# Kernel optimization log

Hardware: AMD Instinct MI355X
Metric: run time of the kernel (lower is better)

Reference implementation:

```python
import jax, jax.numpy as jnp
import numpy as np

WINDOW_SIZE = 11
SIGMA = 1.5
CHANNELS = 3
WEIGHT = 0.1
DATA_RANGE = 1.0


def _gaussian_kernel(window_size, sigma, channels):
    coords = jnp.arange(window_size, dtype=jnp.float32) - window_size // 2
    g = jnp.exp(-coords ** 2 / (2.0 * sigma ** 2))
    g = g / g.sum()
    k2d = jnp.outer(g, g)  # (W, W)
    # OIHW depthwise kernel: (channels, 1, W, W)
    return jnp.tile(k2d[None, None, :, :], (channels, 1, 1, 1))


def _dwconv(x, window):
    pad = WINDOW_SIZE // 2
    return jax.lax.conv_general_dilated(
        x, window,
        window_strides=(1, 1),
        padding=[(pad, pad), (pad, pad)],
        dimension_numbers=("NCHW", "OIHW", "NCHW"),
        feature_group_count=CHANNELS,
    )


def setup_inputs() -> dict:
    key = jax.random.key(0)
    k1, k2 = jax.random.split(key)
    shape = (16, 3, 512, 512)
    pred = jax.random.uniform(k1, shape, dtype=jnp.float32)
    target = jax.random.uniform(k2, shape, dtype=jnp.float32)
    window = _gaussian_kernel(WINDOW_SIZE, SIGMA, CHANNELS)
    return {"pred": pred, "target": target, "window": window}


def reference(pred, target, window):
    C1 = (0.01 * DATA_RANGE) ** 2
    C2 = (0.03 * DATA_RANGE) ** 2
    mu1 = _dwconv(pred, window)
    mu2 = _dwconv(target, window)
    mu1_sq = mu1 * mu1
    mu2_sq = mu2 * mu2
    mu1_mu2 = mu1 * mu2
    sigma1_sq = _dwconv(pred * pred, window) - mu1_sq
    sigma2_sq = _dwconv(target * target, window) - mu2_sq
    sigma12 = _dwconv(pred * target, window) - mu1_mu2
    numerator = (2.0 * mu1_mu2 + C1) * (2.0 * sigma12 + C2)
    denominator = (mu1_sq + mu2_sq + C1) * (sigma1_sq + sigma2_sq + C2)
    ssim_val = jnp.mean(numerator / denominator)
    return WEIGHT * (1.0 - ssim_val)
```

## Files before the change

### kernel.cpp

```cpp
#include <hip/hip_runtime.h>

typedef _Float16 half8 __attribute__((ext_vector_type(8)));
typedef _Float16 half4 __attribute__((ext_vector_type(4)));
typedef float f32x4 __attribute__((ext_vector_type(4)));

#define W 512
#define H 512
#define NPIX (16.0f*3.0f*512.0f*512.0f)
#define NACC 64
#define TPSTR 88
#define TPL (64*TPSTR)
#define ROWF 84
#define TOFF 6720
#define SFLOATS 13568
#define NT 12
#define NSLOT 7
#define NINST 53

#define VMCNT0() asm volatile("s_waitcnt vmcnt(0)" ::: "memory")
#define LGKM0()  asm volatile("s_waitcnt lgkmcnt(0)" ::: "memory")
#define BAR()    { asm volatile("" ::: "memory"); __builtin_amdgcn_s_barrier(); asm volatile("" ::: "memory"); }

__global__ __launch_bounds__(512) void ssim_main(const float* __restrict__ pred,
                                                 const float* __restrict__ targ,
                                                 const float* __restrict__ win,
                                                 float* __restrict__ ws) {
    const int tid  = threadIdx.x;
    const int lane = tid & 63;
    const int wv   = tid >> 6;
    const int lo   = lane & 15;
    const int hi   = lane >> 4;

    float* acc = ws;
    const float* zp = ws + 64;

    __shared__ __align__(16) float stageA[SFLOATS];
    __shared__ __align__(16) float stageB[SFLOATS];
    __shared__ __align__(16) _Float16 TP[4 * TPL];
    __shared__ _Float16 gw[64];
    __shared__ float wsum[8];

    if (tid < 64) {
        const int d = tid - 18;
        float val = 0.f;
        if (d >= 0 && d <= 10)
            val = win[55 + d] * __builtin_amdgcn_rcpf(sqrtf(win[60]));
        gw[tid] = (_Float16)val;
    }
    __syncthreads();

    half8 Bw;
    #pragma unroll
    for (int j = 0; j < 8; ++j)
        Bw[j] = gw[15 + hi * 8 + j - lo];

    int prow[NSLOT], pcol[NSLOT], parr[NSLOT];
    #pragma unroll
    for (int s = 0; s < NSLOT; ++s) {
        const int inst = s * 8 + wv;
        const int id   = inst * 64 + lane;
        const int arr  = (id >= 1680) ? 1 : 0;
        const int cid  = id - arr * 1680;
        const int r    = (cid * 3121) >> 16;
        const int cc   = cid - r * 21;
        const bool bad = (r >= 80) || (cc >= 20);
        prow[s] = bad ? 0x100000 : r;
        pcol[s] = cc * 4 - 8;
        parr[s] = arr;
    }

    const int b  = (blockIdx.x & 7) * 32 + (blockIdx.x >> 3);
    const int t0 = b * NT;
    float sum = 0.f;
    const f32x4 zero4 = {0.f, 0.f, 0.f, 0.f};
    const float C1 = 1e-4f, C2 = 9e-4f;

#define STAGE(tidx, BUF)                                                       \
    {                                                                          \
        const int nc = (tidx) >> 6, rem = (tidx) & 63;                         \
        const int y0 = (rem >> 3) * 64, x0 = (rem & 7) * 64;                   \
        const float* P  = pred + (size_t)nc * (W * H);                         \
        const float* Tt = targ + (size_t)nc * (W * H);                         \
        _Pragma("unroll")                                                      \
        for (int s = 0; s < NSLOT; ++s) {                                      \
            const int inst = s * 8 + wv;                                       \
            if (inst < NINST) {                                                \
                const int gy = y0 - 8 + prow[s];                               \
                const int gx = x0 + pcol[s];                                   \
                const bool ok = ((unsigned)gy < H) && ((unsigned)gx < W);      \
                const float* bp  = parr[s] ? Tt : P;                           \
                const float* src = ok ? (bp + (gy * W + gx)) : zp;             \
                __builtin_amdgcn_global_load_lds(                              \
                    (const __attribute__((address_space(1))) void*)src,        \
                    (__attribute__((address_space(3))) void*)&BUF[inst * 256], \
                    16, 0, 0);                                                 \
            }                                                                  \
        }                                                                      \
        __builtin_amdgcn_sched_barrier(0);            \
    }

#define COMPUTE(BUF)                                                           \
    {                                                                          \
        _Pragma("unroll")                                                      \
        for (int it = 0; it < 3; ++it) {                                       \
            const int t = wv + it * 8;                                         \
            if (t < 20) {                                                      \
                const int rt = t >> 2, ct = t & 3;                             \
                const int row  = rt * 16 + lo;                                 \
                const int coff = ct * 16 + hi * 8;                             \
                const float* SP = &BUF[row * ROWF + coff];                     \
                float pf[8], tf[8];                                            \
                *(float4*)&pf[0] = *(const float4*)SP;                         \
                *(float4*)&pf[4] = *(const float4*)(SP + 4);                   \
                *(float4*)&tf[0] = *(const float4*)(SP + TOFF);                \
                *(float4*)&tf[4] = *(const float4*)(SP + TOFF + 4);            \
                half8 pa, ta, qa, xa;                                          \
                _Pragma("unroll")                                              \
                for (int j = 0; j < 8; ++j) {                                  \
                    const float p = pf[j], t2 = tf[j];                         \
                    pa[j] = (_Float16)p;                                       \
                    ta[j] = (_Float16)t2;                                      \
                    qa[j] = (_Float16)fmaf(t2, t2, p * p);                     \
                    xa[j] = (_Float16)(p * t2);                                \
                }                                                              \
                const f32x4 d0 = __builtin_amdgcn_mfma_f32_16x16x32_f16(pa, Bw, zero4, 0, 0, 0); \
                const f32x4 d1 = __builtin_amdgcn_mfma_f32_16x16x32_f16(ta, Bw, zero4, 0, 0, 0); \
                const f32x4 d2 = __builtin_amdgcn_mfma_f32_16x16x32_f16(qa, Bw, zero4, 0, 0, 0); \
                const f32x4 d3 = __builtin_amdgcn_mfma_f32_16x16x32_f16(xa, Bw, zero4, 0, 0, 0); \
                const int tbase = (ct * 16 + lo) * TPSTR + rt * 16 + hi * 4;   \
                half4 h0, h1, h2, h3;                                          \
                _Pragma("unroll")                                              \
                for (int r = 0; r < 4; ++r) {                                  \
                    h0[r] = (_Float16)d0[r]; h1[r] = (_Float16)d1[r];          \
                    h2[r] = (_Float16)d2[r]; h3[r] = (_Float16)d3[r];          \
                }                                                              \
                *(half4*)&TP[0 * TPL + tbase] = h0;                            \
                *(half4*)&TP[1 * TPL + tbase] = h1;                            \
                *(half4*)&TP[2 * TPL + tbase] = h2;                            \
                *(half4*)&TP[3 * TPL + tbase] = h3;                            \
            }                                                                  \
        }                                                                      \
        LGKM0(); BAR();                                                        \
        _Pragma("unroll")                                                      \
        for (int iv = 0; iv < 2; ++iv) {                                       \
            const int v = wv + iv * 8;                                         \
            const int rtv = v >> 2, ct = v & 3;                                \
            const int abase = (ct * 16 + lo) * TPSTR + rtv * 16 + hi * 8;      \
            const half8 a0 = *(const half8*)&TP[0 * TPL + abase];              \
            const half8 a1 = *(const half8*)&TP[1 * TPL + abase];              \
            const half8 a2 = *(const half8*)&TP[2 * TPL + abase];              \
            const half8 a3 = *(const half8*)&TP[3 * TPL + abase];              \
            const f32x4 m1 = __builtin_amdgcn_mfma_f32_16x16x32_f16(a0, Bw, zero4, 0, 0, 0); \
            const f32x4 m2 = __builtin_amdgcn_mfma_f32_16x16x32_f16(a1, Bw, zero4, 0, 0, 0); \
            const f32x4 qq = __builtin_amdgcn_mfma_f32_16x16x32_f16(a2, Bw, zero4, 0, 0, 0); \
            const f32x4 pt = __builtin_amdgcn_mfma_f32_16x16x32_f16(a3, Bw, zero4, 0, 0, 0); \
            _Pragma("unroll")                                                  \
            for (int r = 0; r < 4; ++r) {                                      \
                const float mu1 = m1[r], mu2 = m2[r];                          \
                const float ms  = fmaf(mu1, mu1, mu2 * mu2);                   \
                const float m12 = mu1 * mu2;                                   \
                const float s12 = pt[r] - m12;                                 \
                const float ssm = qq[r] - ms;                                  \
                const float num = fmaf(2.f, m12, C1) * fmaf(2.f, s12, C2);     \
                const float den = (ms + C1) * (ssm + C2);                      \
                sum += num * __builtin_amdgcn_rcpf(den);                       \
            }                                                                  \
        }                                                                      \
    }

    STAGE(t0, stageA);
    VMCNT0(); BAR();

    #pragma unroll 1
    for (int i = 0; i < NT; i += 2) {
        STAGE(t0 + i + 1, stageB);
        COMPUTE(stageA);
        VMCNT0(); BAR();
        if (i + 2 < NT) STAGE(t0 + i + 2, stageA);
        COMPUTE(stageB);
        VMCNT0(); BAR();
    }

    #pragma unroll
    for (int off = 32; off > 0; off >>= 1) sum += __shfl_down(sum, off, 64);
    if (lane == 0) wsum[wv] = sum;
    __syncthreads();
    if (tid == 0) {
        float bs = 0.f;
        #pragma unroll
        for (int w2 = 0; w2 < 8; ++w2) bs += wsum[w2];
        atomicAdd(&acc[blockIdx.x & (NACC - 1)], bs);
    }
#undef STAGE
#undef COMPUTE
}

__global__ void ssim_final(const float* __restrict__ acc, float* __restrict__ out) {
    float s = 0.f;
    #pragma unroll
    for (int i = 0; i < NACC; ++i) s += acc[i];
    out[0] = 0.1f * (1.0f - s / NPIX);
}

extern "C" void kernel_launch(void* const* d_in, const int* in_sizes, int n_in,
                              void* d_out, int out_size, void* d_ws, size_t ws_size,
                              hipStream_t stream) {
    const float* pred = (const float*)d_in[0];
    const float* targ = (const float*)d_in[1];
    const float* win  = (const float*)d_in[2];
    float* out = (float*)d_out;
    float* ws  = (float*)d_ws;

    hipMemsetAsync(ws, 0, 512, stream);
    ssim_main<<<256, 512, 0, stream>>>(pred, targ, win, ws);
    ssim_final<<<1, 1, 0, stream>>>(ws, out);
}
```

Before: 40.62 us.

## Halve tile width to 64x32, use 256-thread blocks and 512 blocks

```diff
diff --git a/kernel.cpp b/kernel.cpp
--- a/kernel.cpp
+++ b/kernel.cpp
@@ -8,20 +8,19 @@
 #define H 512
 #define NPIX (16.0f*3.0f*512.0f*512.0f)
 #define NACC 64
-#define TPSTR 88
-#define TPL (64*TPSTR)
-#define ROWF 84
-#define TOFF 6720
-#define SFLOATS 13568
+#define AFL 3696
+#define SFL 7424
+#define NINST 29
+#define TPSTR 80
+#define TPL 2560
 #define NT 12
-#define NSLOT 7
-#define NINST 53
 
 #define VMCNT0() asm volatile("s_waitcnt vmcnt(0)" ::: "memory")
 #define LGKM0()  asm volatile("s_waitcnt lgkmcnt(0)" ::: "memory")
 #define BAR()    { asm volatile("" ::: "memory"); __builtin_amdgcn_s_barrier(); asm volatile("" ::: "memory"); }
-
-__global__ __launch_bounds__(512) void ssim_main(const float* __restrict__ pred,
+#define MFMA(A,B) __builtin_amdgcn_mfma_f32_16x16x32_f16((A),(B),zero4,0,0,0)
+
+__global__ __launch_bounds__(256) void ssim_main(const float* __restrict__ pred,
                                                  const float* __restrict__ targ,
                                                  const float* __restrict__ win,
                                                  float* __restrict__ ws) {
@@ -34,11 +33,10 @@
     float* acc = ws;
     const float* zp = ws + 64;
 
-    __shared__ __align__(16) float stageA[SFLOATS];
-    __shared__ __align__(16) float stageB[SFLOATS];
-    __shared__ __align__(16) _Float16 TP[4 * TPL];
+    __shared__ float stageA[SFL];
+    __shared__ float stageB[SFL];
+    __shared__ _Float16 TP[4 * TPL];
     __shared__ _Float16 gw[64];
-    __shared__ float wsum[8];
 
     if (tid < 64) {
         const int d = tid - 18;
@@ -47,49 +45,50 @@
             val = win[55 + d] * __builtin_amdgcn_rcpf(sqrtf(win[60]));
         gw[tid] = (_Float16)val;
     }
-    __syncthreads();
-
-    half8 Bw;
-    #pragma unroll
-    for (int j = 0; j < 8; ++j)
-        Bw[j] = gw[15 + hi * 8 + j - lo];
-
-    int prow[NSLOT], pcol[NSLOT], parr[NSLOT];
-    #pragma unroll
-    for (int s = 0; s < NSLOT; ++s) {
-        const int inst = s * 8 + wv;
+    {
+        const half4 z4 = {(_Float16)0.f, (_Float16)0.f, (_Float16)0.f, (_Float16)0.f};
+        #pragma unroll
+        for (int i = 0; i < 10; ++i)
+            *(half4*)&TP[(i * 256 + tid) * 4] = z4;
+    }
+
+    int prow[8], pcol[8], parr[8];
+    #pragma unroll
+    for (int s = 0; s < 8; ++s) {
+        const int inst = s * 4 + wv;
         const int id   = inst * 64 + lane;
-        const int arr  = (id >= 1680) ? 1 : 0;
-        const int cid  = id - arr * 1680;
-        const int r    = (cid * 3121) >> 16;
-        const int cc   = cid - r * 21;
-        const bool bad = (r >= 80) || (cc >= 20);
-        prow[s] = bad ? 0x100000 : r;
+        const bool okid = (id < 1848);
+        const int arr  = (id >= 924 && okid) ? 1 : 0;
+        const int cid  = id - 924 * arr;
+        const int r    = (cid * 5462) >> 16;
+        const int cc   = cid - r * 12;
+        prow[s] = okid ? r : (1 << 20);
         pcol[s] = cc * 4 - 8;
         parr[s] = arr;
     }
 
-    const int b  = (blockIdx.x & 7) * 32 + (blockIdx.x >> 3);
-    const int t0 = b * NT;
-    float sum = 0.f;
     const f32x4 zero4 = {0.f, 0.f, 0.f, 0.f};
     const float C1 = 1e-4f, C2 = 9e-4f;
+    float sum = 0.f;
+
+    const int bsw = (blockIdx.x & 7) * 64 + (blockIdx.x >> 3);
+    const int t0  = bsw * NT;
 
 #define STAGE(tidx, BUF)                                                       \
     {                                                                          \
-        const int nc = (tidx) >> 6, rem = (tidx) & 63;                         \
-        const int y0 = (rem >> 3) * 64, x0 = (rem & 7) * 64;                   \
-        const float* P  = pred + (size_t)nc * (W * H);                         \
-        const float* Tt = targ + (size_t)nc * (W * H);                         \
+        const int nc = (tidx) >> 7, rem = (tidx) & 127;                        \
+        const int y0 = (rem >> 4) * 64, x0 = (rem & 15) * 32;                  \
+        const float* Pb = pred + (size_t)nc * (W * H);                         \
+        const float* Tb = targ + (size_t)nc * (W * H);                         \
         _Pragma("unroll")                                                      \
-        for (int s = 0; s < NSLOT; ++s) {                                      \
-            const int inst = s * 8 + wv;                                       \
-            if (inst < NINST) {                                                \
+        for (int s = 0; s < 8; ++s) {                                          \
+            const int inst = s * 4 + wv;                                       \
+            if (inst < NINST) {                              \
                 const int gy = y0 - 8 + prow[s];                               \
                 const int gx = x0 + pcol[s];                                   \
                 const bool ok = ((unsigned)gy < H) && ((unsigned)gx < W);      \
-                const float* bp  = parr[s] ? Tt : P;                           \
-                const float* src = ok ? (bp + (gy * W + gx)) : zp;             \
+                const float* bp  = parr[s] ? Tb : Pb;                          \
+                const float* src = ok ? (bp + ((size_t)gy * W + gx)) : zp;     \
                 __builtin_amdgcn_global_load_lds(                              \
                     (const __attribute__((address_space(1))) void*)src,        \
                     (__attribute__((address_space(3))) void*)&BUF[inst * 256], \
@@ -103,57 +102,61 @@
     {                                                                          \
         _Pragma("unroll")                                                      \
         for (int it = 0; it < 3; ++it) {                                       \
-            const int t = wv + it * 8;                                         \
-            if (t < 20) {                                                      \
-                const int rt = t >> 2, ct = t & 3;                             \
-                const int row  = rt * 16 + lo;                                 \
-                const int coff = ct * 16 + hi * 8;                             \
-                const float* SP = &BUF[row * ROWF + coff];                     \
+            const int t = wv + it * 4;                                         \
+            if (t < 10) {                                    \
+                const int rt = t >> 1, ct = t & 1;                             \
+                const float* SP = &BUF[(rt * 16 + lo) * 48 + ct * 16 + hi * 8];\
                 float pf[8], tf[8];                                            \
-                *(float4*)&pf[0] = *(const float4*)SP;                         \
-                *(float4*)&pf[4] = *(const float4*)(SP + 4);                   \
-                *(float4*)&tf[0] = *(const float4*)(SP + TOFF);                \
-                *(float4*)&tf[4] = *(const float4*)(SP + TOFF + 4);            \
-                half8 pa, ta, qa, xa;                                          \
+                *(f32x4*)&pf[0] = *(const f32x4*)SP;                           \
+                *(f32x4*)&pf[4] = *(const f32x4*)(SP + 4);                     \
+                *(f32x4*)&tf[0] = *(const f32x4*)(SP + AFL);                   \
+                *(f32x4*)&tf[4] = *(const f32x4*)(SP + AFL + 4);               \
+                half8 pa, ta;                                                  \
                 _Pragma("unroll")                                              \
                 for (int j = 0; j < 8; ++j) {                                  \
-                    const float p = pf[j], t2 = tf[j];                         \
-                    pa[j] = (_Float16)p;                                       \
-                    ta[j] = (_Float16)t2;                                      \
-                    qa[j] = (_Float16)fmaf(t2, t2, p * p);                     \
-                    xa[j] = (_Float16)(p * t2);                                \
+                    pa[j] = (_Float16)pf[j];                                   \
+                    ta[j] = (_Float16)tf[j];                                   \
                 }                                                              \
-                const f32x4 d0 = __builtin_amdgcn_mfma_f32_16x16x32_f16(pa, Bw, zero4, 0, 0, 0); \
-                const f32x4 d1 = __builtin_amdgcn_mfma_f32_16x16x32_f16(ta, Bw, zero4, 0, 0, 0); \
-                const f32x4 d2 = __builtin_amdgcn_mfma_f32_16x16x32_f16(qa, Bw, zero4, 0, 0, 0); \
-                const f32x4 d3 = __builtin_amdgcn_mfma_f32_16x16x32_f16(xa, Bw, zero4, 0, 0, 0); \
-                const int tbase = (ct * 16 + lo) * TPSTR + rt * 16 + hi * 4;   \
-                half4 h0, h1, h2, h3;                                          \
-                _Pragma("unroll")                                              \
-                for (int r = 0; r < 4; ++r) {                                  \
-                    h0[r] = (_Float16)d0[r]; h1[r] = (_Float16)d1[r];          \
-                    h2[r] = (_Float16)d2[r]; h3[r] = (_Float16)d3[r];          \
+                const half8 qa = pa * pa + ta * ta;                            \
+                const half8 xa = pa * ta;                                      \
+                const f32x4 d0 = MFMA(pa, Bw);                                 \
+                const f32x4 d1 = MFMA(ta, Bw);                                 \
+                const f32x4 d2 = MFMA(qa, Bw);                                 \
+                const f32x4 d3 = MFMA(xa, Bw);                                 \
+                const int tb = (ct * 16 + lo) * TPSTR + rt * 16 + hi * 4;      \
+                if (rt == 4 && hi == 3) {          \
+                    TP[0 * TPL + tb] = (_Float16)d0[0];                        \
+                    TP[1 * TPL + tb] = (_Float16)d1[0];                        \
+                    TP[2 * TPL + tb] = (_Float16)d2[0];                        \
+                    TP[3 * TPL + tb] = (_Float16)d3[0];                        \
+                } else {                                                       \
+                    half4 h0, h1, h2, h3;                                      \
+                    _Pragma("unroll")                                          \
+                    for (int r = 0; r < 4; ++r) {                              \
+                        h0[r] = (_Float16)d0[r]; h1[r] = (_Float16)d1[r];      \
+                        h2[r] = (_Float16)d2[r]; h3[r] = (_Float16)d3[r];      \
+                    }                                                          \
+                    *(half4*)&TP[0 * TPL + tb] = h0;                           \
+                    *(half4*)&TP[1 * TPL + tb] = h1;                           \
+                    *(half4*)&TP[2 * TPL + tb] = h2;                           \
+                    *(half4*)&TP[3 * TPL + tb] = h3;                           \
                 }                                                              \
-                *(half4*)&TP[0 * TPL + tbase] = h0;                            \
-                *(half4*)&TP[1 * TPL + tbase] = h1;                            \
-                *(half4*)&TP[2 * TPL + tbase] = h2;                            \
-                *(half4*)&TP[3 * TPL + tbase] = h3;                            \
             }                                                                  \
         }                                                                      \
-        LGKM0(); BAR();                                                        \
+        LGKM0(); BAR();                      \
         _Pragma("unroll")                                                      \
         for (int iv = 0; iv < 2; ++iv) {                                       \
-            const int v = wv + iv * 8;                                         \
-            const int rtv = v >> 2, ct = v & 3;                                \
-            const int abase = (ct * 16 + lo) * TPSTR + rtv * 16 + hi * 8;      \
-            const half8 a0 = *(const half8*)&TP[0 * TPL + abase];              \
-            const half8 a1 = *(const half8*)&TP[1 * TPL + abase];              \
-            const half8 a2 = *(const half8*)&TP[2 * TPL + abase];              \
-            const half8 a3 = *(const half8*)&TP[3 * TPL + abase];              \
-            const f32x4 m1 = __builtin_amdgcn_mfma_f32_16x16x32_f16(a0, Bw, zero4, 0, 0, 0); \
-            const f32x4 m2 = __builtin_amdgcn_mfma_f32_16x16x32_f16(a1, Bw, zero4, 0, 0, 0); \
-            const f32x4 qq = __builtin_amdgcn_mfma_f32_16x16x32_f16(a2, Bw, zero4, 0, 0, 0); \
-            const f32x4 pt = __builtin_amdgcn_mfma_f32_16x16x32_f16(a3, Bw, zero4, 0, 0, 0); \
+            const int v = wv + iv * 4;                                         \
+            const int rtv = v >> 1, ct = v & 1;                                \
+            const int ah = (ct * 16 + lo) * TPSTR + rtv * 16 + hi * 8;         \
+            const half8 a0 = *(const half8*)&TP[0 * TPL + ah];                 \
+            const half8 a1 = *(const half8*)&TP[1 * TPL + ah];                 \
+            const half8 a2 = *(const half8*)&TP[2 * TPL + ah];                 \
+            const half8 a3 = *(const half8*)&TP[3 * TPL + ah];                 \
+            const f32x4 m1 = MFMA(a0, Bw);                                     \
+            const f32x4 m2 = MFMA(a1, Bw);                                     \
+            const f32x4 qq = MFMA(a2, Bw);                                     \
+            const f32x4 pt = MFMA(a3, Bw);                                     \
             _Pragma("unroll")                                                  \
             for (int r = 0; r < 4; ++r) {                                      \
                 const float mu1 = m1[r], mu2 = m2[r];                          \
@@ -169,7 +172,12 @@
     }
 
     STAGE(t0, stageA);
-    VMCNT0(); BAR();
+    LGKM0(); VMCNT0(); BAR();
+
+    half8 Bw;
+    #pragma unroll
+    for (int j = 0; j < 8; ++j)
+        Bw[j] = gw[15 + hi * 8 + j - lo];
 
     #pragma unroll 1
     for (int i = 0; i < NT; i += 2) {
@@ -183,14 +191,8 @@
 
     #pragma unroll
     for (int off = 32; off > 0; off >>= 1) sum += __shfl_down(sum, off, 64);
-    if (lane == 0) wsum[wv] = sum;
-    __syncthreads();
-    if (tid == 0) {
-        float bs = 0.f;
-        #pragma unroll
-        for (int w2 = 0; w2 < 8; ++w2) bs += wsum[w2];
-        atomicAdd(&acc[blockIdx.x & (NACC - 1)], bs);
-    }
+    if (lane == 0)
+        atomicAdd(&acc[(blockIdx.x * 4 + wv) & (NACC - 1)], sum);
 #undef STAGE
 #undef COMPUTE
 }
@@ -212,6 +214,6 @@
     float* ws  = (float*)d_ws;
 
     hipMemsetAsync(ws, 0, 512, stream);
-    ssim_main<<<256, 512, 0, stream>>>(pred, targ, win, ws);
+    ssim_main<<<512, 256, 0, stream>>>(pred, targ, win, ws);
     ssim_final<<<1, 1, 0, stream>>>(ws, out);
 }
```

Result: slower. 53.48 us (+31.6%).
